# Optimization experiments

Hardware: AMD Instinct MI355X
Metric: run time of the kernel (lower is better)

The kernel has to match this reference:

```python
import jax, jax.numpy as jnp
import numpy as np

T, D, DI, E, K = 8192, 512, 256, 8, 2  # tokens, in_features, d_intermediate, n_routed_experts, top_k


def setup_inputs() -> dict:
    key = jax.random.key(0)
    k1, k2, k3, k4 = jax.random.split(key, 4)
    x = jax.random.normal(k1, (T, D), jnp.float32)
    # Gate linear weight (nn.Linear(in_features, n_routed_experts, bias=False))
    wg = jax.random.normal(k2, (E, D), jnp.float32) / np.sqrt(D).astype(np.float32)
    # fc1: [E, 2*d_intermediate, in_features] / sqrt(in_features)
    fc1 = jax.random.normal(k3, (E, 2 * DI, D), jnp.float32) / np.sqrt(D).astype(np.float32)
    # fc2: [E, in_features, d_intermediate] / sqrt(d_intermediate)
    fc2 = jax.random.normal(k4, (E, D, DI), jnp.float32) / np.sqrt(DI).astype(np.float32)
    return {"x": x, "wg": wg, "fc1": fc1, "fc2": fc2}


def reference(x, wg, fc1, fc2):
    route_scale = 1.0
    T_, D_ = x.shape
    E_ = fc1.shape[0]
    # --- Gate: softmax scores -> top-k routing weights / expert indices ---
    scores = jax.nn.softmax(x @ wg.T, axis=-1)            # [T, E]
    weights, indices = jax.lax.top_k(scores, K)           # [T, K]
    weights = weights * route_scale
    # --- Routed experts: per (token, activated-expert) pair ---
    idx_flat = indices.reshape(-1)                        # [T*K] expert id per pair
    x_pairs = jnp.repeat(x, K, axis=0)                    # [T*K, D] (pair p -> token p//K)
    out_pairs = jnp.zeros_like(x_pairs)
    for e in range(E_):                                   # fixed small expert loop
        h = x_pairs @ fc1[e].T                            # [T*K, 2*DI]
        y, gate = jnp.split(h, 2, axis=-1)                # chunk(2, dim=-1)
        o = (y * jax.nn.silu(gate)) @ fc2[e].T            # [T*K, D]
        out_pairs = out_pairs + jnp.where((idx_flat == e)[:, None], o, 0.0)
    # combine: z[t] = sum_k weights[t,k] * out_pairs[t,k]  (torch.bmm(weights[:,None], x_by_expert))
    z = jnp.einsum('tk,tkd->td', weights, out_pairs.reshape(T_, K, D_))
    return z
```

## Files before the change

kernel.cpp:

```cpp
#include <hip/hip_runtime.h>
#include <hip/hip_bf16.h>
#include <stdint.h>

#define T_TOK 8192
#define D_IN  512
#define DINT  256
#define NE    8

typedef float f32x4 __attribute__((ext_vector_type(4)));
typedef short bf16x8 __attribute__((ext_vector_type(8)));
typedef unsigned short u16;
typedef unsigned short u16x4 __attribute__((ext_vector_type(4)));

#define WS_CNT   0
#define WS_WP    1024
#define WS_BT    66560
#define WS_F2B   197632
#define WS_F1B   2294784
#define WS_XB    6489088
#define WS_AS    14877696
#define WS_OG    23725056

typedef const __attribute__((address_space(1))) void* gptr_t;
typedef __attribute__((address_space(3))) void* lptr_t;
#define GLL16(g, s) __builtin_amdgcn_global_load_lds((gptr_t)(g), (lptr_t)(s), 16, 0, 0)

static __device__ __forceinline__ u16 f32_bf16(float f) {
    union { float f; uint32_t u; } v; v.f = f;
    uint32_t u = v.u;
    uint32_t r = (u + 0x7FFFu + ((u >> 16) & 1u)) >> 16;
    return (u16)r;
}
static __device__ __forceinline__ float bf16_f32(u16 h) {
    union { uint32_t u; float f; } v; v.u = ((uint32_t)h) << 16; return v.f;
}

__global__ __launch_bounds__(256) void cvt_kernel(
    const float* __restrict__ fc1, const float* __restrict__ fc2,
    u16* __restrict__ f1s, u16* __restrict__ f2s, int* __restrict__ cnt)
{
    if (blockIdx.x == 0 && threadIdx.x < NE) cnt[threadIdx.x] = 0;
    const int C1 = NE * 4 * 16 * 512;
    const int C2 = NE * 4 * 8 * 512;
    for (int c = blockIdx.x * 256 + threadIdx.x; c < C1 + C2; c += gridDim.x * 256) {
        const float* s; u16* d;
        if (c < C1) {
            int lane = c & 63, f = (c >> 6) & 7, ks = (c >> 9) & 15, p = c >> 13;
            int e = p >> 2, nt = p & 3;
            int row = ((f < 4) ? (nt * 64 + f * 16) : (256 + nt * 64 + (f - 4) * 16)) + (lane & 15);
            int k = ks * 32 + (lane >> 4) * 8;
            s = fc1 + (size_t)e * 512 * 512 + (size_t)row * 512 + k;
            d = f1s + (size_t)c * 8;
        } else {
            int c2 = c - C1;
            int lane = c2 & 63, f = (c2 >> 6) & 7, ks = (c2 >> 9) & 7, p = c2 >> 12;
            int e = p >> 2, nt = p & 3;
            int row = nt * 128 + f * 16 + (lane & 15);
            int k = ks * 32 + (lane >> 4) * 8;
            s = fc2 + (size_t)e * 512 * 256 + (size_t)row * 256 + k;
            d = f2s + (size_t)c2 * 8;
        }
        float4 v0 = *(const float4*)s;
        float4 v1 = *(const float4*)(s + 4);
        bf16x8 o;
        o[0] = (short)f32_bf16(v0.x); o[1] = (short)f32_bf16(v0.y);
        o[2] = (short)f32_bf16(v0.z); o[3] = (short)f32_bf16(v0.w);
        o[4] = (short)f32_bf16(v1.x); o[5] = (short)f32_bf16(v1.y);
        o[6] = (short)f32_bf16(v1.z); o[7] = (short)f32_bf16(v1.w);
        *(bf16x8*)d = o;
    }
}

__global__ __launch_bounds__(256) void gate_kernel(
    const float* __restrict__ x, const float* __restrict__ wg,
    int* __restrict__ cnt, u16* __restrict__ bt, float* __restrict__ wpair,
    u16* __restrict__ xb)
{
    __shared__ float wgl[NE * D_IN];
    __shared__ float xt[64][67];
    __shared__ float part[256 * 9];
    __shared__ int ecnt[NE];
    __shared__ int gbase[NE];

    const int tid = threadIdx.x;
    const int t0  = blockIdx.x * 64;
    const int tl  = tid & 63;
    const int kq  = tid >> 6;

    for (int i = tid; i < NE * D_IN; i += 256) wgl[i] = wg[i];
    if (tid < NE) ecnt[tid] = 0;

    float acc[NE];
#pragma unroll
    for (int e = 0; e < NE; e++) acc[e] = 0.f;

    for (int c = 0; c < 8; ++c) {
        __syncthreads();
#pragma unroll
        for (int i = 0; i < 4; ++i) {
            int idx = i * 256 + tid;
            int row = idx >> 4, c4 = idx & 15;
            float4 v = *(const float4*)&x[(size_t)(t0 + row) * D_IN + c * 64 + c4 * 4];
            u16x4 o;
            o.x = f32_bf16(v.x); o.y = f32_bf16(v.y);
            o.z = f32_bf16(v.z); o.w = f32_bf16(v.w);
            *(u16x4*)&xb[(size_t)(t0 + row) * D_IN + c * 64 + c4 * 4] = o;
            xt[c4 * 4 + 0][row] = v.x; xt[c4 * 4 + 1][row] = v.y;
            xt[c4 * 4 + 2][row] = v.z; xt[c4 * 4 + 3][row] = v.w;
        }
        __syncthreads();
#pragma unroll
        for (int j = 0; j < 16; ++j) {
            float xv = xt[kq * 16 + j][tl];
#pragma unroll
            for (int e = 0; e < NE; e++)
                acc[e] = fmaf(xv, wgl[e * D_IN + c * 64 + kq * 16 + j], acc[e]);
        }
    }
#pragma unroll
    for (int e = 0; e < NE; e++) part[tid * 9 + e] = acc[e];
    __syncthreads();

    int i1 = 0, i2 = -1, lp1 = 0, lp2 = 0;
    if (tid < 64) {
        float s8[NE];
#pragma unroll
        for (int e = 0; e < NE; e++)
            s8[e] = part[tid * 9 + e] + part[(64 + tid) * 9 + e]
                  + part[(128 + tid) * 9 + e] + part[(192 + tid) * 9 + e];
        float m = s8[0];
#pragma unroll
        for (int e = 1; e < NE; e++) m = fmaxf(m, s8[e]);
        float p[NE], s = 0.f;
#pragma unroll
        for (int e = 0; e < NE; e++) { p[e] = expf(s8[e] - m); s += p[e]; }
        float inv = 1.f / s;
        float v1 = p[0];
#pragma unroll
        for (int e = 1; e < NE; e++) if (p[e] > v1) { v1 = p[e]; i1 = e; }
        float v2 = -1.f;
#pragma unroll
        for (int e = 0; e < NE; e++) if (e != i1 && p[e] > v2) { v2 = p[e]; i2 = e; }
        int t = t0 + tid;
        wpair[2 * t]     = v1 * inv;
        wpair[2 * t + 1] = v2 * inv;
        lp1 = atomicAdd(&ecnt[i1], 1);
        lp2 = atomicAdd(&ecnt[i2], 1);
    }
    __syncthreads();
    if (tid < NE) gbase[tid] = atomicAdd(&cnt[tid], ecnt[tid]);
    __syncthreads();
    if (tid < 64) {
        int t = t0 + tid;
        bt[i1 * T_TOK + gbase[i1] + lp1] = (u16)(2 * t);
        bt[i2 * T_TOK + gbase[i2] + lp2] = (u16)(2 * t + 1);
    }
}

__global__ __launch_bounds__(256) void fc1_kernel(
    const u16* __restrict__ xb, const u16* __restrict__ f1s,
    const int* __restrict__ cnt, const u16* __restrict__ bt,
    u16* __restrict__ acts)
{
    __shared__ __align__(16) u16 shm[16384];
    __shared__ u16 slot_l[128];

    const int bid = blockIdx.x;
    const int e   = bid & 7;
    const int nt  = (bid >> 3) & 3;
    const int mt  = bid >> 5;
    const int n   = cnt[e];
    const int row0 = mt * 128;
    if (row0 >= n) return;

    int tpre = 0;
#pragma unroll
    for (int ee = 0; ee < NE; ++ee)
        if (ee < e) tpre += (cnt[ee] + 127) >> 7;

    const int tid = threadIdx.x;
    const int wv  = tid >> 6, lane = tid & 63;
    const int l15 = lane & 15, lhi = lane >> 4;
    const int wr  = wv >> 1, wc = wv & 1;

    if (tid < 128) {
        int r = row0 + tid;
        slot_l[tid] = bt[e * T_TOK + ((r < n) ? r : (n - 1))];
    }
    __syncthreads();

    u16* asl = shm;
    u16* bsl = shm + 8192;

    const u16* srcA0 = xb + (size_t)(slot_l[(wv * 2 + 0) * 16 + l15] >> 1) * D_IN + lhi * 8;
    const u16* srcA1 = xb + (size_t)(slot_l[(wv * 2 + 1) * 16 + l15] >> 1) * D_IN + lhi * 8;
    const int fb0 = wv * 2, fb1 = wv * 2 + 1;
    const u16* srcB0 = f1s + (size_t)(e * 4 + nt) * 65536 + fb0 * 512 + lane * 8;
    const u16* srcB1 = f1s + (size_t)(e * 4 + nt) * 65536 + fb1 * 512 + lane * 8;

    f32x4 acc[4][4];
#pragma unroll
    for (int m = 0; m < 4; m++)
#pragma unroll
        for (int nb = 0; nb < 4; nb++) acc[m][nb] = (f32x4)0.f;

    GLL16(srcA0, &asl[0 * 4096 + fb0 * 512]);
    GLL16(srcA1, &asl[0 * 4096 + fb1 * 512]);
    GLL16(srcB0, &bsl[0 * 4096 + fb0 * 512]);
    GLL16(srcB1, &bsl[0 * 4096 + fb1 * 512]);
    __syncthreads();

#pragma unroll
    for (int ks = 0; ks < 16; ++ks) {
        const int cur = ks & 1;
        if (ks < 15) {
            GLL16(srcA0 + (ks + 1) * 32,   &asl[(cur ^ 1) * 4096 + fb0 * 512]);
            GLL16(srcA1 + (ks + 1) * 32,   &asl[(cur ^ 1) * 4096 + fb1 * 512]);
            GLL16(srcB0 + (ks + 1) * 4096, &bsl[(cur ^ 1) * 4096 + fb0 * 512]);
            GLL16(srcB1 + (ks + 1) * 4096, &bsl[(cur ^ 1) * 4096 + fb1 * 512]);
        }
        bf16x8 a[4], b[4];
#pragma unroll
        for (int m = 0; m < 4; m++)
            a[m] = *(const bf16x8*)&asl[cur * 4096 + (wr * 4 + m) * 512 + lane * 8];
        b[0] = *(const bf16x8*)&bsl[cur * 4096 + (wc * 2 + 0) * 512 + lane * 8];
        b[1] = *(const bf16x8*)&bsl[cur * 4096 + (wc * 2 + 1) * 512 + lane * 8];
        b[2] = *(const bf16x8*)&bsl[cur * 4096 + (4 + wc * 2 + 0) * 512 + lane * 8];
        b[3] = *(const bf16x8*)&bsl[cur * 4096 + (4 + wc * 2 + 1) * 512 + lane * 8];
#pragma unroll
        for (int m = 0; m < 4; m++)
#pragma unroll
            for (int nb = 0; nb < 4; nb++)
                acc[m][nb] = __builtin_amdgcn_mfma_f32_16x16x32_bf16(
                    a[m], b[nb], acc[m][nb], 0, 0, 0);
        __syncthreads();
    }

#pragma unroll
    for (int m = 0; m < 4; m++) {
#pragma unroll
        for (int j = 0; j < 4; j++) {
            int row = wr * 64 + m * 16 + lhi * 4 + j;
#pragma unroll
            for (int q = 0; q < 2; q++) {
                float y = acc[m][q][j], g = acc[m][q + 2][j];
                float v = y * g / (1.f + __expf(-g));
                shm[row * 72 + wc * 32 + q * 16 + l15] = f32_bf16(v);
            }
        }
    }
    __syncthreads();

    u16* tile = acts + (size_t)(tpre + mt) * 32768;
#pragma unroll
    for (int i = 0; i < 4; ++i) {
        int c = wv * 4 + i;
        int mf = c >> 1, ksr = c & 1;
        bf16x8 v = *(const bf16x8*)&shm[(mf * 16 + l15) * 72 + ksr * 32 + lhi * 8];
        *(bf16x8*)&tile[(2 * nt + ksr) * 4096 + mf * 512 + lane * 8] = v;
    }
}

__global__ __launch_bounds__(256) void fc2_kernel(
    const u16* __restrict__ acts, const u16* __restrict__ f2s,
    const int* __restrict__ cnt, const u16* __restrict__ bt,
    u16* __restrict__ og)
{
    __shared__ __align__(16) u16 asl[2][8 * 512];
    __shared__ __align__(16) u16 bsl[2][8 * 512];
    __shared__ u16 slot_l[128];

    const int bid = blockIdx.x;
    const int e   = bid & 7;
    const int nt  = (bid >> 3) & 3;
    const int mt  = bid >> 5;
    const int n   = cnt[e];
    const int row0 = mt * 128;
    if (row0 >= n) return;

    int tpre = 0;
#pragma unroll
    for (int ee = 0; ee < NE; ++ee)
        if (ee < e) tpre += (cnt[ee] + 127) >> 7;

    const int tid = threadIdx.x;
    const int wv  = tid >> 6, lane = tid & 63;
    const int l15 = lane & 15, lhi = lane >> 4;
    const int wr  = wv >> 1, wc = wv & 1;

    if (tid < 128) {
        int r = row0 + tid;
        slot_l[tid] = bt[e * T_TOK + ((r < n) ? r : (n - 1))];
    }
    __syncthreads();

    const int fb0 = wv * 2, fb1 = wv * 2 + 1;
    const u16* srcA0 = acts + (size_t)(tpre + mt) * 32768 + fb0 * 512 + lane * 8;
    const u16* srcA1 = acts + (size_t)(tpre + mt) * 32768 + fb1 * 512 + lane * 8;
    const u16* srcB0 = f2s + (size_t)(e * 4 + nt) * 32768 + fb0 * 512 + lane * 8;
    const u16* srcB1 = f2s + (size_t)(e * 4 + nt) * 32768 + fb1 * 512 + lane * 8;

    f32x4 acc[4][4];
#pragma unroll
    for (int m = 0; m < 4; m++)
#pragma unroll
        for (int nb = 0; nb < 4; nb++) acc[m][nb] = (f32x4)0.f;

    GLL16(srcA0, &asl[0][fb0 * 512]);
    GLL16(srcA1, &asl[0][fb1 * 512]);
    GLL16(srcB0, &bsl[0][fb0 * 512]);
    GLL16(srcB1, &bsl[0][fb1 * 512]);
    __syncthreads();

#pragma unroll
    for (int ks = 0; ks < 8; ++ks) {
        const int cur = ks & 1;
        if (ks < 7) {
            GLL16(srcA0 + (ks + 1) * 4096, &asl[cur ^ 1][fb0 * 512]);
            GLL16(srcA1 + (ks + 1) * 4096, &asl[cur ^ 1][fb1 * 512]);
            GLL16(srcB0 + (ks + 1) * 4096, &bsl[cur ^ 1][fb0 * 512]);
            GLL16(srcB1 + (ks + 1) * 4096, &bsl[cur ^ 1][fb1 * 512]);
        }
        bf16x8 a[4], b[4];
#pragma unroll
        for (int m = 0; m < 4; m++)
            a[m] = *(const bf16x8*)&asl[cur][(wr * 4 + m) * 512 + lane * 8];
#pragma unroll
        for (int nb = 0; nb < 4; nb++)
            b[nb] = *(const bf16x8*)&bsl[cur][(wc * 4 + nb) * 512 + lane * 8];
#pragma unroll
        for (int m = 0; m < 4; m++)
#pragma unroll
            for (int nb = 0; nb < 4; nb++)
                acc[m][nb] = __builtin_amdgcn_mfma_f32_16x16x32_bf16(
                    a[m], b[nb], acc[m][nb], 0, 0, 0);
        __syncthreads();
    }

#pragma unroll
    for (int m = 0; m < 4; m++) {
#pragma unroll
        for (int j = 0; j < 4; j++) {
            int lrow = wr * 64 + m * 16 + lhi * 4 + j;
            if (row0 + lrow < n) {
                int slot = slot_l[lrow];
                u16* dst = og + (size_t)slot * D_IN + nt * 128 + wc * 64 + l15;
#pragma unroll
                for (int nb = 0; nb < 4; nb++)
                    dst[nb * 16] = f32_bf16(acc[m][nb][j]);
            }
        }
    }
}

__global__ __launch_bounds__(256) void combine_kernel(
    const u16* __restrict__ og, const float* __restrict__ wpair,
    float* __restrict__ out)
{
    int idx = blockIdx.x * 256 + threadIdx.x;
    int t  = idx >> 6;
    int c8 = (idx & 63) * 8;
    float w0 = wpair[2 * t], w1 = wpair[2 * t + 1];
    bf16x8 a = *(const bf16x8*)&og[(size_t)(2 * t) * D_IN + c8];
    bf16x8 b = *(const bf16x8*)&og[(size_t)(2 * t + 1) * D_IN + c8];
    float4 o0, o1;
#pragma unroll
    for (int j = 0; j < 4; j++) {
        o0[j] = w0 * bf16_f32((u16)a[j])     + w1 * bf16_f32((u16)b[j]);
        o1[j] = w0 * bf16_f32((u16)a[j + 4]) + w1 * bf16_f32((u16)b[j + 4]);
    }
    float* orow = out + (size_t)t * D_IN + c8;
    *(float4*)orow = o0;
    *(float4*)(orow + 4) = o1;
}

extern "C" void kernel_launch(void* const* d_in, const int* in_sizes, int n_in,
                              void* d_out, int out_size, void* d_ws, size_t ws_size,
                              hipStream_t stream) {
    const float* x   = (const float*)d_in[0];
    const float* wg  = (const float*)d_in[1];
    const float* fc1 = (const float*)d_in[2];
    const float* fc2 = (const float*)d_in[3];
    float* out = (float*)d_out;
    char* ws = (char*)d_ws;

    int*   cnt   = (int*)(ws + WS_CNT);
    float* wpair = (float*)(ws + WS_WP);
    u16*   bt    = (u16*)(ws + WS_BT);
    u16*   f2s   = (u16*)(ws + WS_F2B);
    u16*   f1s   = (u16*)(ws + WS_F1B);
    u16*   xb    = (u16*)(ws + WS_XB);
    u16*   acts  = (u16*)(ws + WS_AS);
    u16*   og    = (u16*)(ws + WS_OG);

    cvt_kernel<<<1024, 256, 0, stream>>>(fc1, fc2, f1s, f2s, cnt);
    gate_kernel<<<T_TOK / 64, 256, 0, stream>>>(x, wg, cnt, bt, wpair, xb);
    fc1_kernel<<<2048, 256, 0, stream>>>(xb, f1s, cnt, bt, acts);
    fc2_kernel<<<2048, 256, 0, stream>>>(acts, f2s, cnt, bt, og);
    combine_kernel<<<T_TOK * (D_IN / 8) / 256, 256, 0, stream>>>(og, wpair, out);
}
```

Baseline: 76.01 us.

## Pre-gather routed token rows into contiguous tiles before fc1 GEMM

Adds a separate gather kernel that copies each expert's routed token rows of bf16 x into contiguous tile-major buffers laid out in MFMA fragment order. fc1 then streams its A operand from this contiguous buffer instead of doing indexed row gathers, and no longer needs the slot lookup and its barrier. The trade-off is an extra kernel launch plus a full write and re-read of the gathered activations, about 16 MB of extra traffic. Each gathered tile is also now read by the four N-tiles from the new buffer rather than from the shared source rows.

New measurement: 79.93 us. 5.1% more time.

```diff
diff --git a/kernel.cpp b/kernel.cpp
--- a/kernel.cpp
+++ b/kernel.cpp
@@ -20,6 +20,7 @@
 #define WS_XB    6489088
 #define WS_AS    14877696
 #define WS_OG    23725056
+#define WS_XG    40502272
 
 typedef const __attribute__((address_space(1))) void* gptr_t;
 typedef __attribute__((address_space(3))) void* lptr_t;
@@ -157,13 +158,41 @@
     }
 }
 
+__global__ __launch_bounds__(256) void xgather_kernel(
+    const u16* __restrict__ xb, const int* __restrict__ cnt,
+    const u16* __restrict__ bt, u16* __restrict__ xg)
+{
+    int tb[NE], tc[NE], tot = 0;
+#pragma unroll
+    for (int e = 0; e < NE; ++e) { tb[e] = tot; tc[e] = (cnt[e] + 127) >> 7; tot += tc[e]; }
+
+    const int lane = threadIdx.x & 63;
+    const int l15 = lane & 15, lhi = lane >> 4;
+    const int wid = (blockIdx.x * 256 + threadIdx.x) >> 6;
+    const int nw  = (gridDim.x * 256) >> 6;
+    const int total = tot * 128;
+
+    for (int task = wid; task < total; task += nw) {
+        int g = task >> 7, sub = task & 127;
+        int ks = sub >> 3, frag = sub & 7;
+        int e = 0;
+#pragma unroll
+        for (int ee = 1; ee < NE; ++ee) if (tb[ee] <= g) e = ee;
+        int mt = g - tb[e];
+        int n = cnt[e];
+        int r = mt * 128 + frag * 16 + l15;
+        if (r >= n) r = n - 1;
+        int slot = bt[e * T_TOK + r];
+        bf16x8 v = *(const bf16x8*)&xb[(size_t)(slot >> 1) * D_IN + ks * 32 + lhi * 8];
+        *(bf16x8*)&xg[(size_t)g * 65536 + ks * 4096 + frag * 512 + lane * 8] = v;
+    }
+}
+
 __global__ __launch_bounds__(256) void fc1_kernel(
-    const u16* __restrict__ xb, const u16* __restrict__ f1s,
-    const int* __restrict__ cnt, const u16* __restrict__ bt,
-    u16* __restrict__ acts)
+    const u16* __restrict__ xg, const u16* __restrict__ f1s,
+    const int* __restrict__ cnt, u16* __restrict__ acts)
 {
     __shared__ __align__(16) u16 shm[16384];
-    __shared__ u16 slot_l[128];
 
     const int bid = blockIdx.x;
     const int e   = bid & 7;
@@ -177,24 +206,19 @@
 #pragma unroll
     for (int ee = 0; ee < NE; ++ee)
         if (ee < e) tpre += (cnt[ee] + 127) >> 7;
+    const int g = tpre + mt;
 
     const int tid = threadIdx.x;
     const int wv  = tid >> 6, lane = tid & 63;
     const int l15 = lane & 15, lhi = lane >> 4;
     const int wr  = wv >> 1, wc = wv & 1;
 
-    if (tid < 128) {
-        int r = row0 + tid;
-        slot_l[tid] = bt[e * T_TOK + ((r < n) ? r : (n - 1))];
-    }
-    __syncthreads();
-
     u16* asl = shm;
     u16* bsl = shm + 8192;
 
-    const u16* srcA0 = xb + (size_t)(slot_l[(wv * 2 + 0) * 16 + l15] >> 1) * D_IN + lhi * 8;
-    const u16* srcA1 = xb + (size_t)(slot_l[(wv * 2 + 1) * 16 + l15] >> 1) * D_IN + lhi * 8;
     const int fb0 = wv * 2, fb1 = wv * 2 + 1;
+    const u16* srcA0 = xg + (size_t)g * 65536 + fb0 * 512 + lane * 8;
+    const u16* srcA1 = xg + (size_t)g * 65536 + fb1 * 512 + lane * 8;
     const u16* srcB0 = f1s + (size_t)(e * 4 + nt) * 65536 + fb0 * 512 + lane * 8;
     const u16* srcB1 = f1s + (size_t)(e * 4 + nt) * 65536 + fb1 * 512 + lane * 8;
 
@@ -214,8 +238,8 @@
     for (int ks = 0; ks < 16; ++ks) {
         const int cur = ks & 1;
         if (ks < 15) {
-            GLL16(srcA0 + (ks + 1) * 32,   &asl[(cur ^ 1) * 4096 + fb0 * 512]);
-            GLL16(srcA1 + (ks + 1) * 32,   &asl[(cur ^ 1) * 4096 + fb1 * 512]);
+            GLL16(srcA0 + (ks + 1) * 4096, &asl[(cur ^ 1) * 4096 + fb0 * 512]);
+            GLL16(srcA1 + (ks + 1) * 4096, &asl[(cur ^ 1) * 4096 + fb1 * 512]);
             GLL16(srcB0 + (ks + 1) * 4096, &bsl[(cur ^ 1) * 4096 + fb0 * 512]);
             GLL16(srcB1 + (ks + 1) * 4096, &bsl[(cur ^ 1) * 4096 + fb1 * 512]);
         }
@@ -243,15 +267,15 @@
             int row = wr * 64 + m * 16 + lhi * 4 + j;
 #pragma unroll
             for (int q = 0; q < 2; q++) {
-                float y = acc[m][q][j], g = acc[m][q + 2][j];
-                float v = y * g / (1.f + __expf(-g));
+                float y = acc[m][q][j], gv = acc[m][q + 2][j];
+                float v = y * gv / (1.f + __expf(-gv));
                 shm[row * 72 + wc * 32 + q * 16 + l15] = f32_bf16(v);
             }
         }
     }
     __syncthreads();
 
-    u16* tile = acts + (size_t)(tpre + mt) * 32768;
+    u16* tile = acts + (size_t)g * 32768;
 #pragma unroll
     for (int i = 0; i < 4; ++i) {
         int c = wv * 4 + i;
@@ -392,10 +416,12 @@
     u16*   xb    = (u16*)(ws + WS_XB);
     u16*   acts  = (u16*)(ws + WS_AS);
     u16*   og    = (u16*)(ws + WS_OG);
+    u16*   xg    = (u16*)(ws + WS_XG);
 
     cvt_kernel<<<1024, 256, 0, stream>>>(fc1, fc2, f1s, f2s, cnt);
     gate_kernel<<<T_TOK / 64, 256, 0, stream>>>(x, wg, cnt, bt, wpair, xb);
-    fc1_kernel<<<2048, 256, 0, stream>>>(xb, f1s, cnt, bt, acts);
+    xgather_kernel<<<1024, 256, 0, stream>>>(xb, cnt, bt, xg);
+    fc1_kernel<<<2048, 256, 0, stream>>>(xg, f1s, cnt, acts);
     fc2_kernel<<<2048, 256, 0, stream>>>(acts, f2s, cnt, bt, og);
     combine_kernel<<<T_TOK * (D_IN / 8) / 256, 256, 0, stream>>>(og, wpair, out);
 }
```
